# Optimization experiments

Hardware: AMD Instinct MI355X
Metric: run time of the kernel (lower is better)

The kernel has to match this reference:

```python
import jax, jax.numpy as jnp
import numpy as np

KERNEL_SIZE = 9  # square structuring element, matches __init__ default
ITERATIONS = 1


def setup_inputs() -> dict:
    key = jax.random.key(0)
    label = jax.random.uniform(key, (16, 1024, 1024, 1), dtype=jnp.float32)
    return {"label": label}


def reference(label):
    # cv2.dilate with np.ones((k,k)) == sliding-window max over a k x k square.
    # Default morphology border value for dilate is -inf, so SAME padding with
    # -inf init reproduces cv2's border behavior exactly.
    out = label
    for _ in range(ITERATIONS):
        out = jax.lax.reduce_window(
            out,
            -jnp.inf,
            jax.lax.max,
            window_dimensions=(1, KERNEL_SIZE, KERNEL_SIZE, 1),
            window_strides=(1, 1, 1, 1),
            padding="SAME",
        )
    # Original layer wraps the result in K.stop_gradient.
    return jax.lax.stop_gradient(out)
```

## Files before the change

### kernel.cpp

```cpp
#include <hip/hip_runtime.h>
#include <math.h>

#define IMG  1024
#define ROWS 32

__device__ __forceinline__ float4 max4(const float4 a, const float4 b) {
    return make_float4(fmaxf(a.x, b.x), fmaxf(a.y, b.y),
                       fmaxf(a.z, b.z), fmaxf(a.w, b.w));
}

__global__ __launch_bounds__(256) void dilate9x9(const float* __restrict__ in,
                                                 float* __restrict__ out) {
    const int x0 = threadIdx.x << 2;
    const int y0 = blockIdx.x * ROWS;
    const int b  = blockIdx.y;

    const float* img  = in  + (size_t)b * IMG * IMG;
    float*       oimg = out + (size_t)b * IMG * IMG;

    const bool hasL = (x0 >= 4);
    const bool hasR = (x0 <= IMG - 8);

    auto load_hmax = [&](int iy) -> float4 {
        if (iy < 0 || iy >= IMG)
            return make_float4(-INFINITY, -INFINITY, -INFINITY, -INFINITY);
        const float4* p = reinterpret_cast<const float4*>(img + (size_t)iy * IMG + x0);
        const float4 v1 = p[0];
        const float4 v0 = hasL ? p[-1] : make_float4(-INFINITY, -INFINITY, -INFINITY, -INFINITY);
        const float4 v2 = hasR ? p[ 1] : make_float4(-INFINITY, -INFINITY, -INFINITY, -INFINITY);
        const float a0=v0.x,a1=v0.y,a2=v0.z,a3=v0.w;
        const float a4=v1.x,a5=v1.y,a6=v1.z,a7=v1.w;
        const float a8=v2.x,a9=v2.y,a10=v2.z,a11=v2.w;
        const float core = fmaxf(fmaxf(fmaxf(a3,a4),fmaxf(a5,a6)),fmaxf(a7,a8));
        const float p12  = fmaxf(a1,a2);
        const float p012 = fmaxf(a0,p12);
        const float q910 = fmaxf(a9,a10);
        const float q911 = fmaxf(q910,a11);
        float4 r;
        r.x = fmaxf(core, p012);
        r.y = fmaxf(core, fmaxf(p12,a9));
        r.z = fmaxf(core, fmaxf(a2,q910));
        r.w = fmaxf(core, q911);
        return r;
    };

    float4 C[8];
    #pragma unroll
    for (int j = 0; j < 8; ++j) C[j] = load_hmax(y0 - 4 + j);

    #pragma unroll
    for (int c = 0; c < ROWS / 8; ++c) {
        const int r0 = y0 + (c << 3);
        float4 S[8];
        S[7] = C[7];
        #pragma unroll
        for (int j = 6; j >= 0; --j) S[j] = max4(C[j], S[j + 1]);
        float4 P;
        #pragma unroll
        for (int t = 0; t < 8; ++t) {
            const float4 H = load_hmax(r0 + 4 + t);
            P = (t == 0) ? H : max4(P, H);
            *reinterpret_cast<float4*>(oimg + (size_t)(r0 + t) * IMG + x0) = max4(S[t], P);
            C[t] = H;
        }
    }
}

extern "C" void kernel_launch(void* const* d_in, const int* in_sizes, int n_in,
                              void* d_out, int out_size, void* d_ws, size_t ws_size,
                              hipStream_t stream) {
    const float* in  = (const float*)d_in[0];
    float*       out = (float*)d_out;
    const int B = in_sizes[0] / (IMG * IMG);
    dim3 grid(IMG / ROWS, B);
    dilate9x9<<<grid, 256, 0, stream>>>(in, out);
}
```

Before: 35.30 us.

## Batch unconditional row loads ahead of compute and halve rows per block

Row loads are made branch-free by clamping out-of-range row and column addresses and masking the results afterwards. This lets all 24 float4 loads for an 8-row chunk be issued before any max computation, raising memory-level parallelism. Rows per block drop from 32 to 16, doubling the grid and the share of halo rows re-read. The batched loads also increase register pressure.

```diff
diff --git a/kernel.cpp b/kernel.cpp
--- a/kernel.cpp
+++ b/kernel.cpp
@@ -2,11 +2,26 @@
 #include <math.h>
 
 #define IMG  1024
-#define ROWS 32
+#define ROWS 16
+
+#define NEG4 make_float4(-INFINITY, -INFINITY, -INFINITY, -INFINITY)
 
 __device__ __forceinline__ float4 max4(const float4 a, const float4 b) {
     return make_float4(fmaxf(a.x, b.x), fmaxf(a.y, b.y),
                        fmaxf(a.z, b.z), fmaxf(a.w, b.w));
+}
+
+__device__ __forceinline__ float4 hmax9(const float4 v0, const float4 v1, const float4 v2) {
+    const float core = fmaxf(fmaxf(fmaxf(v0.w, v1.x), fmaxf(v1.y, v1.z)),
+                             fmaxf(v1.w, v2.x));
+    const float p12  = fmaxf(v0.y, v0.z);
+    const float q910 = fmaxf(v2.y, v2.z);
+    float4 r;
+    r.x = fmaxf(core, fmaxf(v0.x, p12));
+    r.y = fmaxf(core, fmaxf(p12, v2.y));
+    r.z = fmaxf(core, fmaxf(v0.z, q910));
+    r.w = fmaxf(core, fmaxf(q910, v2.w));
+    return r;
 }
 
 __global__ __launch_bounds__(256) void dilate9x9(const float* __restrict__ in,
@@ -21,44 +36,57 @@
     const bool hasL = (x0 >= 4);
     const bool hasR = (x0 <= IMG - 8);
 
-    auto load_hmax = [&](int iy) -> float4 {
-        if (iy < 0 || iy >= IMG)
-            return make_float4(-INFINITY, -INFINITY, -INFINITY, -INFINITY);
-        const float4* p = reinterpret_cast<const float4*>(img + (size_t)iy * IMG + x0);
-        const float4 v1 = p[0];
-        const float4 v0 = hasL ? p[-1] : make_float4(-INFINITY, -INFINITY, -INFINITY, -INFINITY);
-        const float4 v2 = hasR ? p[ 1] : make_float4(-INFINITY, -INFINITY, -INFINITY, -INFINITY);
-        const float a0=v0.x,a1=v0.y,a2=v0.z,a3=v0.w;
-        const float a4=v1.x,a5=v1.y,a6=v1.z,a7=v1.w;
-        const float a8=v2.x,a9=v2.y,a10=v2.z,a11=v2.w;
-        const float core = fmaxf(fmaxf(fmaxf(a3,a4),fmaxf(a5,a6)),fmaxf(a7,a8));
-        const float p12  = fmaxf(a1,a2);
-        const float p012 = fmaxf(a0,p12);
-        const float q910 = fmaxf(a9,a10);
-        const float q911 = fmaxf(q910,a11);
-        float4 r;
-        r.x = fmaxf(core, p012);
-        r.y = fmaxf(core, fmaxf(p12,a9));
-        r.z = fmaxf(core, fmaxf(a2,q910));
-        r.w = fmaxf(core, q911);
-        return r;
-    };
+    float4 C[8];
 
-    float4 C[8];
-    #pragma unroll
-    for (int j = 0; j < 8; ++j) C[j] = load_hmax(y0 - 4 + j);
+    {
+        float4 L0[8], L1[8], L2[8];
+        bool   val[8];
+        #pragma unroll
+        for (int j = 0; j < 8; ++j) {
+            const int iy = y0 - 4 + j;
+            val[j] = (iy >= 0);
+            const int cy = val[j] ? iy : 0;
+            const float4* p = reinterpret_cast<const float4*>(img + (size_t)cy * IMG + x0);
+            L1[j] = p[0];
+            L0[j] = *(hasL ? p - 1 : p);
+            L2[j] = *(hasR ? p + 1 : p);
+        }
+        #pragma unroll
+        for (int j = 0; j < 8; ++j) {
+            const float4 l0 = hasL ? L0[j] : NEG4;
+            const float4 l2 = hasR ? L2[j] : NEG4;
+            C[j] = val[j] ? hmax9(l0, L1[j], l2) : NEG4;
+        }
+    }
 
     #pragma unroll
     for (int c = 0; c < ROWS / 8; ++c) {
         const int r0 = y0 + (c << 3);
+
+        float4 L0[8], L1[8], L2[8];
+        bool   val[8];
+        #pragma unroll
+        for (int j = 0; j < 8; ++j) {
+            const int iy = r0 + 4 + j;
+            val[j] = (iy < IMG);
+            const int cy = val[j] ? iy : IMG - 1;
+            const float4* p = reinterpret_cast<const float4*>(img + (size_t)cy * IMG + x0);
+            L1[j] = p[0];
+            L0[j] = *(hasL ? p - 1 : p);
+            L2[j] = *(hasR ? p + 1 : p);
+        }
+
         float4 S[8];
         S[7] = C[7];
         #pragma unroll
         for (int j = 6; j >= 0; --j) S[j] = max4(C[j], S[j + 1]);
+
         float4 P;
         #pragma unroll
         for (int t = 0; t < 8; ++t) {
-            const float4 H = load_hmax(r0 + 4 + t);
+            const float4 l0 = hasL ? L0[t] : NEG4;
+            const float4 l2 = hasR ? L2[t] : NEG4;
+            const float4 H  = val[t] ? hmax9(l0, L1[t], l2) : NEG4;
             P = (t == 0) ? H : max4(P, H);
             *reinterpret_cast<float4*>(oimg + (size_t)(r0 + t) * IMG + x0) = max4(S[t], P);
             C[t] = H;
```

New measurement: 31.25 us. 1.13x faster.
